# Kernel optimization log

Hardware: AMD Instinct MI355X
Metric: run time of the kernel (lower is better)

The kernel has to match this reference:

```python
import jax, jax.numpy as jnp
import numpy as np

B, S, I, C, N = 8, 50, 20, 64, 4096  # batch, max seq len, items per set, channels, num_items


def setup_inputs() -> dict:
    key = jax.random.key(0)
    k1, k2, k3, k4, k5 = jax.random.split(key, 5)
    input_tensor = jax.random.normal(k1, (B, S, I, C), dtype=jnp.float32)
    items_id = jax.random.randint(k2, (B, S, I), 0, N)
    # seq lengths in [1, S] (original truncates each user's sequence)
    batch_seq_length = jax.random.randint(k3, (B,), 1, S + 1)
    items_embedding = jax.random.normal(k4, (N, C), dtype=jnp.float32) * 0.02
    proj_w = jax.random.normal(k5, (C, C), dtype=jnp.float32) / jnp.sqrt(jnp.float32(C))
    proj_b = jnp.zeros((C,), dtype=jnp.float32)
    return {
        "input_tensor": input_tensor,
        "items_embedding": items_embedding,
        "proj_w": proj_w,
        "proj_b": proj_b,
        "items_id": items_id,
        "batch_seq_length": batch_seq_length,
    }


def reference(input_tensor, items_embedding, proj_w, proj_b, items_id, batch_seq_length):
    # Dropout layers are identity in eval mode.
    Bb, Ss, Ii, Cc = input_tensor.shape
    Nn = items_embedding.shape[0]

    # valid sequence positions per user: seq_index < batch_seq_length[b]
    seq_mask = (jnp.arange(Ss)[None, :] < batch_seq_length[:, None]).astype(input_tensor.dtype)  # [B,S]
    m = seq_mask[:, :, None]  # [B,S,1], all I item slots valid inside a valid position

    # segment-mean over item occurrences (replaces the Python dict-of-lists + stack/mean)
    flat_ids = (items_id + jnp.arange(Bb)[:, None, None] * Nn).reshape(-1)  # [B*S*I]
    data = (input_tensor * m[..., None]).reshape(-1, Cc)                    # [B*S*I, C]
    sums = jax.ops.segment_sum(data, flat_ids, num_segments=Bb * Nn).reshape(Bb, Nn, Cc)
    counts = jax.ops.segment_sum(jnp.broadcast_to(m, (Bb, Ss, Ii)).reshape(-1),
                                 flat_ids, num_segments=Bb * Nn).reshape(Bb, Nn)
    present = counts > 0                                                    # user's unique historical items
    mean = sums / jnp.maximum(counts, 1.0)[..., None]                       # [B,N,C]

    # attention of all items over the user's unique historical-item embeddings
    scores = jnp.einsum('nc,bmc->bnm', items_embedding, mean)               # [B,N,N]
    scores = jax.nn.leaky_relu(scores, negative_slope=0.2)
    scores = jnp.where(present[:, None, :], scores, jnp.float32(-1e30))     # softmax only over present items
    attn = jax.nn.softmax(scores, axis=-1)
    user_items_embedding = jnp.einsum('bnm,bmc->bnc', attn, mean)           # [B,N,C]

    proj = user_items_embedding @ proj_w.T + proj_b                         # Linear(C,C)
    return (proj * items_embedding[None]).sum(axis=-1)                      # [B,N]
```

## Files before the change

kernel.cpp:

```cpp
#include <hip/hip_runtime.h>

#define Bb 8
#define Ss 50
#define Ii 20
#define Cc 64
#define Nn 4096
#define MAXM 1024
#define POSB (Ss * Ii)

typedef unsigned short ushort_t;
typedef __attribute__((ext_vector_type(8))) short short8;
typedef __attribute__((ext_vector_type(4))) float f32x4;

__device__ inline ushort_t bf16_rn(float x) {
    unsigned u = __float_as_uint(x);
    u = u + 0x7FFFu + ((u >> 16) & 1u);
    return (ushort_t)(u >> 16);
}
__device__ inline float bf16_f(ushort_t h) { return __uint_as_float(((unsigned)h) << 16); }

__global__ __launch_bounds__(1024) void aux_kernel(
    const float* __restrict__ input, const int* __restrict__ ids,
    const int* __restrict__ seqlen, const float* __restrict__ E,
    const float* __restrict__ W, const float* __restrict__ bias,
    int* __restrict__ Mcnt, int* __restrict__ slotHead, int* __restrict__ gnext,
    float* __restrict__ cvec,
    ushort_t* __restrict__ Ehi, ushort_t* __restrict__ Elo,
    ushort_t* __restrict__ Fhi, ushort_t* __restrict__ Flo) {
    __shared__ int smem[5120];
    int tid = threadIdx.x;

    if (blockIdx.x < Bb) {
        int b = blockIdx.x;
        int* head = smem;
        __shared__ int mcnt;
        for (int i = tid; i < Nn; i += 1024) head[i] = -1;
        if (tid == 0) mcnt = 0;
        __syncthreads();
        int P = seqlen[b] * Ii;
        if (tid < P) {
            int id = ids[b * POSB + tid];
            gnext[b * POSB + tid] = atomicExch(&head[id], tid);
        }
        __syncthreads();
        for (int i = tid; i < Nn; i += 1024) {
            int h = head[i];
            if (h >= 0) slotHead[b * MAXM + atomicAdd(&mcnt, 1)] = h;
        }
        __syncthreads();
        if (tid == 0) Mcnt[b] = mcnt;
    } else {
        int pb = blockIdx.x - Bb;
        float* wlds = (float*)smem;
        float* elds = (float*)smem + 4096;
        int n0 = pb * 16;
#pragma unroll
        for (int i = 0; i < 4; i++) wlds[tid + 1024 * i] = W[tid + 1024 * i];
        float ev = E[(size_t)n0 * Cc + tid];
        elds[tid] = ev;
        __syncthreads();
        int nl = tid >> 6, k = tid & 63;
        float acc = 0.f;
#pragma unroll
        for (int c = 0; c < Cc; c++) acc = fmaf(elds[nl * Cc + c], wlds[c * Cc + k], acc);
        size_t o = (size_t)(n0 + nl) * Cc + k;
        ushort_t fh = bf16_rn(acc);
        Fhi[o] = fh; Flo[o] = bf16_rn(acc - bf16_f(fh));
        ushort_t eh = bf16_rn(ev);
        Ehi[o] = eh; Elo[o] = bf16_rn(ev - bf16_f(eh));
        float p = ev * bias[k];
#pragma unroll
        for (int off = 32; off; off >>= 1) p += __shfl_down(p, off);
        if (k == 0) cvec[n0 + nl] = p;
    }
}

__global__ __launch_bounds__(256) void mean_kernel(
    const float* __restrict__ input, const int* __restrict__ slotHead,
    const int* __restrict__ gnext, const int* __restrict__ Mcnt,
    ushort_t* __restrict__ Mhi, ushort_t* __restrict__ Mlo) {
    int w = (blockIdx.x * 256 + threadIdx.x) >> 6;
    int lane = threadIdx.x & 63;
    int b = w >> 10;
    int slot = w & (MAXM - 1);
    if (slot >= Mcnt[b]) return;
    int p = slotHead[b * MAXM + slot];
    float sum = 0.f; int k = 0;
    while (p >= 0) {
        sum += input[((size_t)(b * POSB + p)) * Cc + lane];
        k++;
        p = gnext[b * POSB + p];
    }
    float mv = sum / (float)k;
    ushort_t h = bf16_rn(mv);
    size_t o = ((size_t)(b * MAXM + slot)) * Cc + lane;
    Mhi[o] = h;
    Mlo[o] = bf16_rn(mv - bf16_f(h));
}

#define MFMA(A, B, C) __builtin_amdgcn_mfma_f32_16x16x32_bf16(A, B, C, 0, 0, 0)

__global__ __launch_bounds__(256) void main_kernel(
    const ushort_t* __restrict__ Ehi, const ushort_t* __restrict__ Elo,
    const ushort_t* __restrict__ Fhi, const ushort_t* __restrict__ Flo,
    const ushort_t* __restrict__ Mhi, const ushort_t* __restrict__ Mlo,
    const int* __restrict__ Mcnt, const float* __restrict__ cvec,
    float* __restrict__ out) {
    int idx = blockIdx.x;
    int ntile = idx >> 3;
    int b = (idx + (idx >> 3) + (idx >> 8)) & 7;
    int tid = threadIdx.x;
    int wave = tid >> 6, lane = tid & 63;
    int kq = lane >> 4;
    int n = ntile * 64 + wave * 16 + (lane & 15);

    size_t nb = (size_t)n * Cc + kq * 8;
    short8 Eh0 = *(const short8*)(Ehi + nb),      Eh1 = *(const short8*)(Ehi + nb + 32);
    short8 El0 = *(const short8*)(Elo + nb),      El1 = *(const short8*)(Elo + nb + 32);
    short8 Fh0 = *(const short8*)(Fhi + nb),      Fh1 = *(const short8*)(Fhi + nb + 32);
    short8 Fl0 = *(const short8*)(Flo + nb),      Fl1 = *(const short8*)(Flo + nb + 32);

    int M = Mcnt[b];
    int nmt = (M + 15) >> 4;
    size_t ab = ((size_t)(b * MAXM) + (lane & 15)) * Cc + kq * 8;

    short8 Ah0 = *(const short8*)(Mhi + ab),      Ah1 = *(const short8*)(Mhi + ab + 32);
    short8 Al0 = *(const short8*)(Mlo + ab),      Al1 = *(const short8*)(Mlo + ab + 32);

    float m0 = -1e30f, l = 0.f, av = 0.f;
    int rowg = kq * 4;

#pragma unroll 1
    for (int mt = 0; mt < nmt; mt++) {
        int mtn = (mt + 1 < nmt) ? mt + 1 : mt;
        size_t an = ab + (size_t)mtn * (16 * Cc);
        short8 Nh0 = *(const short8*)(Mhi + an), Nh1 = *(const short8*)(Mhi + an + 32);
        short8 Nl0 = *(const short8*)(Mlo + an), Nl1 = *(const short8*)(Mlo + an + 32);

        f32x4 S = {0.f, 0.f, 0.f, 0.f}, D = {0.f, 0.f, 0.f, 0.f};
        S = MFMA(Ah0, Eh0, S); S = MFMA(Ah1, Eh1, S);
        S = MFMA(Ah0, El0, S); S = MFMA(Ah1, El1, S);
        S = MFMA(Al0, Eh0, S); S = MFMA(Al1, Eh1, S);
        D = MFMA(Ah0, Fh0, D); D = MFMA(Ah1, Fh1, D);
        D = MFMA(Ah0, Fl0, D); D = MFMA(Ah1, Fl1, D);
        D = MFMA(Al0, Fh0, D); D = MFMA(Al1, Fh1, D);

        int mrow = mt * 16 + rowg;
#pragma unroll
        for (int r = 0; r < 4; r++) {
            if (mrow + r < M) {
                float s = S[r];
                float sc = s > 0.f ? s : 0.2f * s;
                float df = D[r];
                float ex = __expf(-fabsf(sc - m0));
                bool sg = sc > m0;
                float p = sg ? 1.f : ex;
                float al = sg ? ex : 1.f;
                m0 = fmaxf(m0, sc);
                l = l * al + p;
                av = av * al + p * df;
            }
        }
        Ah0 = Nh0; Ah1 = Nh1; Al0 = Nl0; Al1 = Nl1;
    }

#pragma unroll
    for (int mask = 16; mask <= 32; mask <<= 1) {
        float m0b = __shfl_xor(m0, mask);
        float lb  = __shfl_xor(l,  mask);
        float avb = __shfl_xor(av, mask);
        float M0 = fmaxf(m0, m0b);
        float w1 = __expf(m0 - M0), w2 = __expf(m0b - M0);
        m0 = M0;
        l  = l * w1 + lb * w2;
        av = av * w1 + avb * w2;
    }
    if (kq == 0) out[b * Nn + n] = av / l + cvec[n];
}

extern "C" void kernel_launch(void* const* d_in, const int* in_sizes, int n_in,
                              void* d_out, int out_size, void* d_ws, size_t ws_size,
                              hipStream_t stream) {
    (void)in_sizes; (void)n_in; (void)out_size; (void)ws_size;
    const float* input  = (const float*)d_in[0];
    const float* E      = (const float*)d_in[1];
    const float* W      = (const float*)d_in[2];
    const float* bias   = (const float*)d_in[3];
    const int*   ids    = (const int*)d_in[4];
    const int*   seqlen = (const int*)d_in[5];
    float* out = (float*)d_out;

    int*      Mcnt     = (int*)d_ws;
    int*      slotHead = Mcnt + 16;
    int*      gnext    = slotHead + Bb * MAXM;
    float*    cvec     = (float*)(gnext + Bb * POSB);
    ushort_t* Mhi      = (ushort_t*)(cvec + Nn);
    ushort_t* Mlo      = Mhi + (size_t)Bb * MAXM * Cc;
    ushort_t* Ehi      = Mlo + (size_t)Bb * MAXM * Cc;
    ushort_t* Elo      = Ehi + (size_t)Nn * Cc;
    ushort_t* Fhi      = Elo + (size_t)Nn * Cc;
    ushort_t* Flo      = Fhi + (size_t)Nn * Cc;

    aux_kernel <<<Bb + Nn / 16, 1024, 0, stream>>>(input, ids, seqlen, E, W, bias,
                                                   Mcnt, slotHead, gnext, cvec,
                                                   Ehi, Elo, Fhi, Flo);
    mean_kernel<<<Bb * MAXM / 4, 256, 0, stream>>>(input, slotHead, gnext, Mcnt, Mhi, Mlo);
    main_kernel<<<Bb * (Nn / 64), 256, 0, stream>>>(Ehi, Elo, Fhi, Flo, Mhi, Mlo,
                                                    Mcnt, cvec, out);
}
```

Baseline: 104.2 us.

## Fuse three kernels into one cooperative kernel with grid-wide syncs

Merges the setup, segment-mean and attention kernels into a single cooperative launch of 256 blocks, separated by grid.sync barriers. Each phase is grid-strided so the fixed grid covers all work. This aims to remove per-launch overhead and inter-kernel gaps. In exchange it caps residency at one 256-thread block per CU and adds grid barrier cost, which may reduce latency hiding in the attention loop.

```diff
diff --git a/kernel.cpp b/kernel.cpp
--- a/kernel.cpp
+++ b/kernel.cpp
@@ -1,4 +1,7 @@
 #include <hip/hip_runtime.h>
+#include <hip/hip_cooperative_groups.h>
+
+namespace cg = cooperative_groups;
 
 #define Bb 8
 #define Ss 50
@@ -7,6 +10,7 @@
 #define Nn 4096
 #define MAXM 1024
 #define POSB (Ss * Ii)
+#define NBLK 256
 
 typedef unsigned short ushort_t;
 typedef __attribute__((ext_vector_type(8))) short short8;
@@ -19,163 +23,171 @@
 }
 __device__ inline float bf16_f(ushort_t h) { return __uint_as_float(((unsigned)h) << 16); }
 
-__global__ __launch_bounds__(1024) void aux_kernel(
+#define MFMA(A, B, C) __builtin_amdgcn_mfma_f32_16x16x32_bf16(A, B, C, 0, 0, 0)
+
+__global__ __launch_bounds__(256) void fused_kernel(
     const float* __restrict__ input, const int* __restrict__ ids,
     const int* __restrict__ seqlen, const float* __restrict__ E,
     const float* __restrict__ W, const float* __restrict__ bias,
     int* __restrict__ Mcnt, int* __restrict__ slotHead, int* __restrict__ gnext,
     float* __restrict__ cvec,
+    ushort_t* __restrict__ Mhi, ushort_t* __restrict__ Mlo,
     ushort_t* __restrict__ Ehi, ushort_t* __restrict__ Elo,
-    ushort_t* __restrict__ Fhi, ushort_t* __restrict__ Flo) {
-    __shared__ int smem[5120];
+    ushort_t* __restrict__ Fhi, ushort_t* __restrict__ Flo,
+    float* __restrict__ out) {
+    cg::grid_group grid = cg::this_grid();
+    __shared__ float smemf[4352];
+    __shared__ int mcnt;
     int tid = threadIdx.x;
-
-    if (blockIdx.x < Bb) {
-        int b = blockIdx.x;
-        int* head = smem;
-        __shared__ int mcnt;
-        for (int i = tid; i < Nn; i += 1024) head[i] = -1;
+    int blk = blockIdx.x;
+    int lane = tid & 63;
+
+    if (blk < Bb) {
+        int b = blk;
+        int* head = (int*)smemf;
+        for (int i = tid; i < Nn; i += 256) head[i] = -1;
         if (tid == 0) mcnt = 0;
         __syncthreads();
         int P = seqlen[b] * Ii;
-        if (tid < P) {
-            int id = ids[b * POSB + tid];
-            gnext[b * POSB + tid] = atomicExch(&head[id], tid);
+        for (int p = tid; p < P; p += 256) {
+            int id = ids[b * POSB + p];
+            gnext[b * POSB + p] = atomicExch(&head[id], p);
         }
         __syncthreads();
-        for (int i = tid; i < Nn; i += 1024) {
+        for (int i = tid; i < Nn; i += 256) {
             int h = head[i];
             if (h >= 0) slotHead[b * MAXM + atomicAdd(&mcnt, 1)] = h;
         }
         __syncthreads();
         if (tid == 0) Mcnt[b] = mcnt;
     } else {
-        int pb = blockIdx.x - Bb;
-        float* wlds = (float*)smem;
-        float* elds = (float*)smem + 4096;
-        int n0 = pb * 16;
-#pragma unroll
-        for (int i = 0; i < 4; i++) wlds[tid + 1024 * i] = W[tid + 1024 * i];
-        float ev = E[(size_t)n0 * Cc + tid];
-        elds[tid] = ev;
-        __syncthreads();
+        int pb = blk - Bb;
+        float* wlds = smemf;
+        float* elds = smemf + 4096;
+        for (int i = tid; i < Cc * Cc; i += 256) wlds[i] = W[i];
         int nl = tid >> 6, k = tid & 63;
-        float acc = 0.f;
-#pragma unroll
-        for (int c = 0; c < Cc; c++) acc = fmaf(elds[nl * Cc + c], wlds[c * Cc + k], acc);
-        size_t o = (size_t)(n0 + nl) * Cc + k;
-        ushort_t fh = bf16_rn(acc);
-        Fhi[o] = fh; Flo[o] = bf16_rn(acc - bf16_f(fh));
-        ushort_t eh = bf16_rn(ev);
-        Ehi[o] = eh; Elo[o] = bf16_rn(ev - bf16_f(eh));
-        float p = ev * bias[k];
-#pragma unroll
-        for (int off = 32; off; off >>= 1) p += __shfl_down(p, off);
-        if (k == 0) cvec[n0 + nl] = p;
+        for (int t = pb; t < Nn / 4; t += NBLK - Bb) {
+            int n0 = t * 4;
+            __syncthreads();
+            float ev = E[(size_t)n0 * Cc + tid];
+            elds[tid] = ev;
+            __syncthreads();
+            float acc = 0.f;
+#pragma unroll
+            for (int c = 0; c < Cc; c++) acc = fmaf(elds[nl * Cc + c], wlds[c * Cc + k], acc);
+            size_t o = (size_t)(n0 + nl) * Cc + k;
+            ushort_t fh = bf16_rn(acc);
+            Fhi[o] = fh; Flo[o] = bf16_rn(acc - bf16_f(fh));
+            ushort_t eh = bf16_rn(ev);
+            Ehi[o] = eh; Elo[o] = bf16_rn(ev - bf16_f(eh));
+            float p = ev * bias[k];
+#pragma unroll
+            for (int off = 32; off; off >>= 1) p += __shfl_down(p, off);
+            if (k == 0) cvec[n0 + nl] = p;
+        }
     }
-}
-
-__global__ __launch_bounds__(256) void mean_kernel(
-    const float* __restrict__ input, const int* __restrict__ slotHead,
-    const int* __restrict__ gnext, const int* __restrict__ Mcnt,
-    ushort_t* __restrict__ Mhi, ushort_t* __restrict__ Mlo) {
-    int w = (blockIdx.x * 256 + threadIdx.x) >> 6;
-    int lane = threadIdx.x & 63;
-    int b = w >> 10;
-    int slot = w & (MAXM - 1);
-    if (slot >= Mcnt[b]) return;
-    int p = slotHead[b * MAXM + slot];
-    float sum = 0.f; int k = 0;
-    while (p >= 0) {
-        sum += input[((size_t)(b * POSB + p)) * Cc + lane];
-        k++;
-        p = gnext[b * POSB + p];
+
+    __threadfence();
+    grid.sync();
+
+    {
+        int w0 = (blk * 256 + tid) >> 6;
+        for (int rep = 0; rep < 8; rep++) {
+            int si = w0 + 1024 * rep;
+            int b = si >> 10;
+            int slot = si & (MAXM - 1);
+            if (slot < Mcnt[b]) {
+                int p = slotHead[b * MAXM + slot];
+                float sum = 0.f; int k = 0;
+                while (p >= 0) {
+                    sum += input[((size_t)(b * POSB + p)) * Cc + lane];
+                    k++;
+                    p = gnext[b * POSB + p];
+                }
+                float mv = sum / (float)k;
+                ushort_t h = bf16_rn(mv);
+                size_t o = ((size_t)(b * MAXM + slot)) * Cc + lane;
+                Mhi[o] = h;
+                Mlo[o] = bf16_rn(mv - bf16_f(h));
+            }
+        }
     }
-    float mv = sum / (float)k;
-    ushort_t h = bf16_rn(mv);
-    size_t o = ((size_t)(b * MAXM + slot)) * Cc + lane;
-    Mhi[o] = h;
-    Mlo[o] = bf16_rn(mv - bf16_f(h));
-}
-
-#define MFMA(A, B, C) __builtin_amdgcn_mfma_f32_16x16x32_bf16(A, B, C, 0, 0, 0)
-
-__global__ __launch_bounds__(256) void main_kernel(
-    const ushort_t* __restrict__ Ehi, const ushort_t* __restrict__ Elo,
-    const ushort_t* __restrict__ Fhi, const ushort_t* __restrict__ Flo,
-    const ushort_t* __restrict__ Mhi, const ushort_t* __restrict__ Mlo,
-    const int* __restrict__ Mcnt, const float* __restrict__ cvec,
-    float* __restrict__ out) {
-    int idx = blockIdx.x;
-    int ntile = idx >> 3;
-    int b = (idx + (idx >> 3) + (idx >> 8)) & 7;
-    int tid = threadIdx.x;
-    int wave = tid >> 6, lane = tid & 63;
+
+    __threadfence();
+    grid.sync();
+
+    int wave = tid >> 6;
     int kq = lane >> 4;
-    int n = ntile * 64 + wave * 16 + (lane & 15);
-
-    size_t nb = (size_t)n * Cc + kq * 8;
-    short8 Eh0 = *(const short8*)(Ehi + nb),      Eh1 = *(const short8*)(Ehi + nb + 32);
-    short8 El0 = *(const short8*)(Elo + nb),      El1 = *(const short8*)(Elo + nb + 32);
-    short8 Fh0 = *(const short8*)(Fhi + nb),      Fh1 = *(const short8*)(Fhi + nb + 32);
-    short8 Fl0 = *(const short8*)(Flo + nb),      Fl1 = *(const short8*)(Flo + nb + 32);
-
-    int M = Mcnt[b];
-    int nmt = (M + 15) >> 4;
-    size_t ab = ((size_t)(b * MAXM) + (lane & 15)) * Cc + kq * 8;
-
-    short8 Ah0 = *(const short8*)(Mhi + ab),      Ah1 = *(const short8*)(Mhi + ab + 32);
-    short8 Al0 = *(const short8*)(Mlo + ab),      Al1 = *(const short8*)(Mlo + ab + 32);
-
-    float m0 = -1e30f, l = 0.f, av = 0.f;
     int rowg = kq * 4;
-
 #pragma unroll 1
-    for (int mt = 0; mt < nmt; mt++) {
-        int mtn = (mt + 1 < nmt) ? mt + 1 : mt;
-        size_t an = ab + (size_t)mtn * (16 * Cc);
-        short8 Nh0 = *(const short8*)(Mhi + an), Nh1 = *(const short8*)(Mhi + an + 32);
-        short8 Nl0 = *(const short8*)(Mlo + an), Nl1 = *(const short8*)(Mlo + an + 32);
-
-        f32x4 S = {0.f, 0.f, 0.f, 0.f}, D = {0.f, 0.f, 0.f, 0.f};
-        S = MFMA(Ah0, Eh0, S); S = MFMA(Ah1, Eh1, S);
-        S = MFMA(Ah0, El0, S); S = MFMA(Ah1, El1, S);
-        S = MFMA(Al0, Eh0, S); S = MFMA(Al1, Eh1, S);
-        D = MFMA(Ah0, Fh0, D); D = MFMA(Ah1, Fh1, D);
-        D = MFMA(Ah0, Fl0, D); D = MFMA(Ah1, Fl1, D);
-        D = MFMA(Al0, Fh0, D); D = MFMA(Al1, Fh1, D);
-
-        int mrow = mt * 16 + rowg;
-#pragma unroll
-        for (int r = 0; r < 4; r++) {
-            if (mrow + r < M) {
-                float s = S[r];
-                float sc = s > 0.f ? s : 0.2f * s;
-                float df = D[r];
-                float ex = __expf(-fabsf(sc - m0));
-                bool sg = sc > m0;
-                float p = sg ? 1.f : ex;
-                float al = sg ? ex : 1.f;
-                m0 = fmaxf(m0, sc);
-                l = l * al + p;
-                av = av * al + p * df;
+    for (int rep = 0; rep < 2; rep++) {
+        int idx = rep * NBLK + blk;
+        int ntile = idx >> 3;
+        int b = (idx + (idx >> 3) + (idx >> 8)) & 7;
+        int n = ntile * 64 + wave * 16 + (lane & 15);
+
+        size_t nb = (size_t)n * Cc + kq * 8;
+        short8 Eh0 = *(const short8*)(Ehi + nb), Eh1 = *(const short8*)(Ehi + nb + 32);
+        short8 El0 = *(const short8*)(Elo + nb), El1 = *(const short8*)(Elo + nb + 32);
+        short8 Fh0 = *(const short8*)(Fhi + nb), Fh1 = *(const short8*)(Fhi + nb + 32);
+        short8 Fl0 = *(const short8*)(Flo + nb), Fl1 = *(const short8*)(Flo + nb + 32);
+
+        int M = Mcnt[b];
+        int nmt = (M + 15) >> 4;
+        size_t ab = ((size_t)(b * MAXM) + (lane & 15)) * Cc + kq * 8;
+
+        short8 Ah0 = *(const short8*)(Mhi + ab), Ah1 = *(const short8*)(Mhi + ab + 32);
+        short8 Al0 = *(const short8*)(Mlo + ab), Al1 = *(const short8*)(Mlo + ab + 32);
+
+        float m0 = -1e30f, l = 0.f, av = 0.f;
+
+#pragma unroll 1
+        for (int mt = 0; mt < nmt; mt++) {
+            int mtn = (mt + 1 < nmt) ? mt + 1 : mt;
+            size_t an = ab + (size_t)mtn * (16 * Cc);
+            short8 Nh0 = *(const short8*)(Mhi + an), Nh1 = *(const short8*)(Mhi + an + 32);
+            short8 Nl0 = *(const short8*)(Mlo + an), Nl1 = *(const short8*)(Mlo + an + 32);
+
+            f32x4 S = {0.f, 0.f, 0.f, 0.f}, D = {0.f, 0.f, 0.f, 0.f};
+            S = MFMA(Ah0, Eh0, S); S = MFMA(Ah1, Eh1, S);
+            S = MFMA(Ah0, El0, S); S = MFMA(Ah1, El1, S);
+            S = MFMA(Al0, Eh0, S); S = MFMA(Al1, Eh1, S);
+            D = MFMA(Ah0, Fh0, D); D = MFMA(Ah1, Fh1, D);
+            D = MFMA(Ah0, Fl0, D); D = MFMA(Ah1, Fl1, D);
+            D = MFMA(Al0, Fh0, D); D = MFMA(Al1, Fh1, D);
+
+            int mrow = mt * 16 + rowg;
+#pragma unroll
+            for (int r = 0; r < 4; r++) {
+                if (mrow + r < M) {
+                    float s = S[r];
+                    float sc = s > 0.f ? s : 0.2f * s;
+                    float df = D[r];
+                    float ex = __expf(-fabsf(sc - m0));
+                    bool sg = sc > m0;
+                    float p = sg ? 1.f : ex;
+                    float al = sg ? ex : 1.f;
+                    m0 = fmaxf(m0, sc);
+                    l = l * al + p;
+                    av = av * al + p * df;
+                }
             }
-        }
-        Ah0 = Nh0; Ah1 = Nh1; Al0 = Nl0; Al1 = Nl1;
+            Ah0 = Nh0; Ah1 = Nh1; Al0 = Nl0; Al1 = Nl1;
+        }
+
+#pragma unroll
+        for (int mask = 16; mask <= 32; mask <<= 1) {
+            float m0b = __shfl_xor(m0, mask);
+            float lb  = __shfl_xor(l,  mask);
+            float avb = __shfl_xor(av, mask);
+            float M0 = fmaxf(m0, m0b);
+            float w1 = __expf(m0 - M0), w2 = __expf(m0b - M0);
+            m0 = M0;
+            l  = l * w1 + lb * w2;
+            av = av * w1 + avb * w2;
+        }
+        if (kq == 0) out[b * Nn + n] = av / l + cvec[n];
     }
-
-#pragma unroll
-    for (int mask = 16; mask <= 32; mask <<= 1) {
-        float m0b = __shfl_xor(m0, mask);
-        float lb  = __shfl_xor(l,  mask);
-        float avb = __shfl_xor(av, mask);
-        float M0 = fmaxf(m0, m0b);
-        float w1 = __expf(m0 - M0), w2 = __expf(m0b - M0);
-        m0 = M0;
-        l  = l * w1 + lb * w2;
-        av = av * w1 + avb * w2;
-    }
-    if (kq == 0) out[b * Nn + n] = av / l + cvec[n];
 }
 
 extern "C" void kernel_launch(void* const* d_in, const int* in_sizes, int n_in,
@@ -201,10 +213,11 @@
     ushort_t* Fhi      = Elo + (size_t)Nn * Cc;
     ushort_t* Flo      = Fhi + (size_t)Nn * Cc;
 
-    aux_kernel <<<Bb + Nn / 16, 1024, 0, stream>>>(input, ids, seqlen, E, W, bias,
-                                                   Mcnt, slotHead, gnext, cvec,
-                                                   Ehi, Elo, Fhi, Flo);
-    mean_kernel<<<Bb * MAXM / 4, 256, 0, stream>>>(input, slotHead, gnext, Mcnt, Mhi, Mlo);
-    main_kernel<<<Bb * (Nn / 64), 256, 0, stream>>>(Ehi, Elo, Fhi, Flo, Mhi, Mlo,
-                                                    Mcnt, cvec, out);
+    void* args[] = {
+        (void*)&input, (void*)&ids, (void*)&seqlen, (void*)&E, (void*)&W, (void*)&bias,
+        (void*)&Mcnt, (void*)&slotHead, (void*)&gnext, (void*)&cvec,
+        (void*)&Mhi, (void*)&Mlo, (void*)&Ehi, (void*)&Elo, (void*)&Fhi, (void*)&Flo,
+        (void*)&out
+    };
+    hipLaunchCooperativeKernel((void*)fused_kernel, dim3(NBLK), dim3(256), args, 0, stream);
 }
```

New measurement: 232.0 us. +122.7%, slower.
